# Kernel optimization log

Hardware: AMD Instinct MI355X
Metric: run time of the kernel (lower is better)

The kernel has to match this reference:

```python
import jax, jax.numpy as jnp
import numpy as np
from jax import lax

B, C, H, W = 2, 3, 512, 512
K = 8                 # kernel_size (= value_patch_size)
G = H // K            # token grid = 64
L = G * G             # 4096 tokens
FD = 128              # feature_dim
PD = C * K * K        # 192 rgb patch dim
MD = PD + FD          # 320 matching token dim
DD = 256              # matching_descriptor_dim
TOPK = 16             # attention_top_k (= reranker_top_k)
RH = 128              # reranker hidden
TEMP = 1.0
NEG = -1e9


def _to_tokens(img):
    # [B,C,H,W] -> [B,L,C*K*K], channel-major patch layout (torch unfold order)
    b = img.shape[0]
    x = img.reshape(b, C, G, K, G, K).transpose(0, 2, 4, 1, 3, 5)
    return x.reshape(b, L, PD)


def _from_tokens(tok):
    # inverse of _to_tokens (non-overlapping fold)
    b = tok.shape[0]
    x = tok.reshape(b, G, G, C, K, K).transpose(0, 3, 1, 4, 2, 5)
    return x.reshape(b, C, H, W)


def setup_inputs() -> dict:
    key = jax.random.key(0)
    ks = jax.random.split(key, 9)
    s = lambda d: 1.0 / np.sqrt(d)
    return {
        "image": jax.random.normal(ks[0], (B, C, H, W), jnp.float32),
        "features": jax.random.normal(ks[1], (B, FD, G, G), jnp.float32),
        "token_mask": jax.random.randint(ks[2], (B, L), 0, 2, jnp.int32),
        "W_desc": jax.random.normal(ks[3], (MD, DD), jnp.float32) * s(MD),
        "Wq_rr": jax.random.normal(ks[4], (MD, RH), jnp.float32) * s(MD),
        "Wk_rr": jax.random.normal(ks[5], (MD, RH), jnp.float32) * s(MD),
        "W1": jax.random.normal(ks[6], (2 * RH + 3, RH), jnp.float32) * s(2 * RH + 3),
        "b1": jnp.zeros((RH,), jnp.float32),
        "W2": jax.random.normal(ks[7], (RH, 1), jnp.float32) * s(RH),
        "b2": jnp.zeros((1,), jnp.float32),
    }


def reference(image, features, token_mask, W_desc, Wq_rr, Wk_rr, W1, b1, W2, b2):
    rgb_tok = _to_tokens(image)                                   # [B,L,192]
    feat_tok = features.reshape(B, FD, L).transpose(0, 2, 1)      # [B,L,128]
    match = jnp.concatenate([rgb_tok, feat_tok], axis=-1)          # [B,L,320]

    # stage-1 matching: descriptor GEMM + scaled dot-product logits
    desc = match @ W_desc                                          # [B,L,256]
    scale = 1.0 / (np.sqrt(DD) * TEMP)
    logits = jnp.einsum("bqd,bkd->bqk", desc, desc) * scale        # [B,L,L]
    key_invalid = token_mask.astype(logits.dtype)                  # 1 = hole
    logits = logits + NEG * key_invalid[:, None, :]

    # top-k candidate selection per query token
    top_logits, top_idx = lax.top_k(logits, TOPK)                  # [B,L,TOPK]

    gather = jax.vmap(lambda m, i: m[i])                            # per-batch gather
    cand = gather(match, top_idx)                                  # [B,L,TOPK,320]

    # relative coordinates on the token grid, normalized
    ys, xs = jnp.meshgrid(jnp.arange(G), jnp.arange(G), indexing="ij")
    pos = jnp.stack([ys.reshape(-1), xs.reshape(-1)], -1).astype(jnp.float32) / G  # [L,2]
    rel = pos[top_idx] - pos[None, :, None, :]                      # [B,L,TOPK,2]

    # reranker MLP over (query, candidate) pairs
    qf = match @ Wq_rr                                              # [B,L,RH]
    kf = cand @ Wk_rr                                               # [B,L,TOPK,RH]
    feats = jnp.concatenate(
        [qf[:, :, None, :] * kf,
         jnp.abs(qf[:, :, None, :] - kf),
         top_logits[..., None],
         rel], axis=-1)                                             # [B,L,TOPK,2RH+3]
    score = (jax.nn.gelu(feats @ W1 + b1, approximate=False) @ W2 + b2)[..., 0]
    refined = top_logits + score                                    # [B,L,TOPK]

    weights = jax.nn.softmax(refined, axis=-1)                      # [B,L,TOPK]

    # gather value patches (value_source='rgb') and blend
    vcand = gather(rgb_tok, top_idx)                                # [B,L,TOPK,192]
    out_tok = jnp.einsum("blk,blkp->blp", weights, vcand)           # [B,L,192]
    out_img = _from_tokens(out_tok)                                 # [B,C,H,W]

    # fusion_mode='replace': replace hole pixels, keep valid pixels
    pix_mask = jnp.repeat(jnp.repeat(token_mask.reshape(B, G, G), K, 1), K, 2)
    pix_mask = pix_mask[:, None, :, :]                              # [B,1,H,W]
    return jnp.where(pix_mask > 0, out_img, image)
```

## Files before the change

### kernel.cpp

```cpp
#include <hip/hip_runtime.h>
#include <hip/hip_bf16.h>
#include <math.h>

#define BB 2
#define CC 3
#define HH 512
#define WW 512
#define GG 64
#define LL 4096
#define FDIM 128
#define PDIM 192
#define MDIM 320
#define DDIM 256
#define TOPK 16
#define RHID 128
#define SCALE (1.0f/16.0f)

#define NQ2 8
#define CHK3 1024
#define KB 2
#define TOKG 16
#define TKT 32
#define NQM 4

__global__ void k_copy_init(const float* __restrict__ img, float* __restrict__ out,
                            int* __restrict__ counts) {
    int i = blockIdx.x * blockDim.x + threadIdx.x;
    if (i < 2 * BB) counts[i] = 0;
    int n4 = BB * CC * HH * WW / 4;
    const float4* s = (const float4*)img;
    float4* d = (float4*)out;
    for (int j = i; j < n4; j += gridDim.x * blockDim.x) d[j] = s[j];
}

__global__ void k_build(const float* __restrict__ img, float* __restrict__ match) {
    int bl = blockIdx.x;
    int b = bl >> 12, l = bl & (LL - 1);
    int gy = l >> 6, gx = l & 63;
    int p = threadIdx.x;
    int c = p >> 6, ky = (p >> 3) & 7, kx = p & 7;
    match[(size_t)bl * MDIM + p] =
        img[((b * CC + c) * HH + gy * 8 + ky) * WW + gx * 8 + kx];
}

__global__ __launch_bounds__(256) void k_buildf(const float* __restrict__ feat,
                                                float* __restrict__ match) {
    int b = blockIdx.y;
    int l0 = blockIdx.x * 64;
    __shared__ float tf[FDIM][65];
    int t = threadIdx.x;
    for (int idx = t; idx < FDIM * 64; idx += 256) {
        int f = idx >> 6, ll = idx & 63;
        tf[f][ll] = feat[((size_t)(b * FDIM + f) << 12) + l0 + ll];
    }
    __syncthreads();
    for (int idx = t; idx < 64 * FDIM; idx += 256) {
        int ll = idx >> 7, f = idx & 127;
        match[(size_t)(b * LL + l0 + ll) * MDIM + PDIM + f] = tf[f][ll];
    }
}

__global__ void k_compact(const int* __restrict__ mask, int* __restrict__ qlist,
                          int* __restrict__ klist, int* __restrict__ counts) {
    int bl = blockIdx.x * blockDim.x + threadIdx.x;
    if (bl >= BB * LL) return;
    int b = bl >> 12, l = bl & (LL - 1);
    if (mask[bl] > 0) {
        int s = atomicAdd(&counts[b], 1);
        qlist[b * LL + s] = l;
    } else {
        int s = atomicAdd(&counts[BB + b], 1);
        klist[b * LL + s] = l;
    }
}

__global__ __launch_bounds__(256) void k_gemm2(const float* __restrict__ match,
        const float* __restrict__ Wd, const float* __restrict__ Wq,
        const float* __restrict__ Wk,
        float* __restrict__ desc, float* __restrict__ qkf) {
    __shared__ float sm[TOKG * MDIM];
    int base = blockIdx.x * TOKG;
    int t = threadIdx.x;
    for (int i = t; i < TOKG * MDIM; i += 256) sm[i] = match[(size_t)base * MDIM + i];
    __syncthreads();
    const float4* sm4 = (const float4*)sm;
    const float* W1p = (t < 128) ? Wq : Wk;
    int c1 = t & 127;
    float acc0[TOKG], acc1[TOKG];
#pragma unroll
    for (int tt = 0; tt < TOKG; ++tt) { acc0[tt] = 0.f; acc1[tt] = 0.f; }
    for (int m = 0; m < MDIM; m += 4) {
        float w00 = Wd[(m+0)*DDIM + t], w01 = Wd[(m+1)*DDIM + t];
        float w02 = Wd[(m+2)*DDIM + t], w03 = Wd[(m+3)*DDIM + t];
        float w10 = W1p[(m+0)*RHID + c1], w11 = W1p[(m+1)*RHID + c1];
        float w12 = W1p[(m+2)*RHID + c1], w13 = W1p[(m+3)*RHID + c1];
        int mg = m >> 2;
#pragma unroll
        for (int tt = 0; tt < TOKG; ++tt) {
            float4 s = sm4[tt * (MDIM/4) + mg];
            acc0[tt] += s.x*w00 + s.y*w01 + s.z*w02 + s.w*w03;
            acc1[tt] += s.x*w10 + s.y*w11 + s.z*w12 + s.w*w13;
        }
    }
#pragma unroll
    for (int tt = 0; tt < TOKG; ++tt) {
        desc[(size_t)(base+tt)*DDIM + t] = acc0[tt];
        qkf [(size_t)(base+tt)*DDIM + t] = acc1[tt];
    }
}

__global__ __launch_bounds__(256) void k_gatherkT(const float* __restrict__ desc,
        const int* __restrict__ klist, const int* __restrict__ counts,
        float* __restrict__ kdesc_t) {
    int b = blockIdx.y;
    int vcnt = counts[BB + b];
    int kt = blockIdx.x * TKT;
    if (kt >= vcnt) return;
    int nk = min(TKT, vcnt - kt);
    __shared__ float sm[TKT][DDIM + 1];
    int t = threadIdx.x;
    for (int r = (t >> 6); r < nk; r += 4) {
        int src = klist[b * LL + kt + r];
        const float4* s = (const float4*)(desc + ((size_t)b * LL + src) * DDIM);
        float4 v = s[t & 63];
        int d0 = (t & 63) * 4;
        sm[r][d0] = v.x; sm[r][d0+1] = v.y; sm[r][d0+2] = v.z; sm[r][d0+3] = v.w;
    }
    __syncthreads();
    float* outb = kdesc_t + (size_t)b * DDIM * LL;
    int kk = t & 31;
    for (int d = (t >> 5); d < DDIM; d += 8) {
        if (kk < nk) outb[(size_t)d * LL + kt + kk] = sm[kk][d];
    }
}

__global__ __launch_bounds__(256, 4) void k_topk4(const float* __restrict__ desc,
        const float* __restrict__ kdt,
        const int* __restrict__ qlist, const int* __restrict__ klist,
        const int* __restrict__ counts,
        float* __restrict__ tval2, int* __restrict__ tidx2) {
    int b = blockIdx.z;
    int kb = blockIdx.y;
    int cnt  = counts[b];
    int vcnt = counts[BB + b];
    int i0 = blockIdx.x * NQ2;
    if (i0 >= cnt) return;
    int nq = min(NQ2, cnt - i0);
    int t = threadIdx.x;
    int lane = t & 63, w = t >> 6;

    __shared__ float sq[NQ2 * DDIM];
    __shared__ float lc[NQ2][CHK3];

#pragma unroll
    for (int qi = 0; qi < NQ2; ++qi) {
        int qtok = qlist[b * LL + i0 + min(qi, nq - 1)];
        sq[qi * DDIM + t] = desc[((size_t)b * LL + qtok) * DDIM + t];
    }
    __syncthreads();

    int khalf = (vcnt + 1) >> 1;
    int kstart = kb * khalf;
    int kend = min(vcnt, kstart + khalf);

    float tva = -INFINITY, tvb = -INFINITY;
    int   tia = 0x7fffffff, tib = 0x7fffffff;

    const float4* sq4 = (const float4*)sq;
    const float* kbase = kdt + (size_t)b * DDIM * LL;
    const int* klb = klist + b * LL;

    int nch = (kend > kstart) ? (kend - kstart + CHK3 - 1) / CHK3 : 0;
    for (int ch = 0; ch < nch; ++ch) {
        int base = kstart + ch * CHK3;
        int k0 = base + 4 * t;
        int k0c = min(k0, LL - 4);

        float acc[NQ2][4];
#pragma unroll
        for (int qi = 0; qi < NQ2; ++qi)
#pragma unroll
            for (int r = 0; r < 4; ++r) acc[qi][r] = 0.f;

#pragma unroll 2
        for (int db = 0; db < DDIM / 4; ++db) {
            float4 qv[NQ2];
#pragma unroll
            for (int qi = 0; qi < NQ2; ++qi) qv[qi] = sq4[qi * (DDIM/4) + db];
#pragma unroll
            for (int dd = 0; dd < 4; ++dd) {
                float4 kx = *(const float4*)(kbase + (size_t)(db * 4 + dd) * LL + k0c);
#pragma unroll
                for (int qi = 0; qi < NQ2; ++qi) {
                    float sv = (dd == 0) ? qv[qi].x : (dd == 1) ? qv[qi].y
                             : (dd == 2) ? qv[qi].z : qv[qi].w;
                    acc[qi][0] += sv * kx.x;
                    acc[qi][1] += sv * kx.y;
                    acc[qi][2] += sv * kx.z;
                    acc[qi][3] += sv * kx.w;
                }
            }
        }
        __syncthreads();
#pragma unroll
        for (int qi = 0; qi < NQ2; ++qi) {
            float4 o;
            o.x = (k0 + 0 < kend) ? acc[qi][0] * SCALE : -INFINITY;
            o.y = (k0 + 1 < kend) ? acc[qi][1] * SCALE : -INFINITY;
            o.z = (k0 + 2 < kend) ? acc[qi][2] * SCALE : -INFINITY;
            o.w = (k0 + 3 < kend) ? acc[qi][3] * SCALE : -INFINITY;
            *(float4*)&lc[qi][4 * t] = o;
        }
        __syncthreads();

        for (int j = 0; j < CHK3 / 64; ++j) {
            int p = j * 64 + lane;
            int gk = base + p;
            int kidx = (gk < kend) ? klb[gk] : 0x7fffffff;
            float va = lc[2 * w + 0][p];
            float vb = lc[2 * w + 1][p];
            {
                float thrv = __shfl(tva, 15);
                int   thri = __shfl(tia, 15);
                bool pass = (va > thrv) || (va == thrv && kidx < thri);
                unsigned long long mball = __ballot(pass);
                while (mball) {
                    int src = __ffsll(mball) - 1;
                    float vv = __shfl(va, src);
                    int   ii = __shfl(kidx, src);
                    bool beat = (vv > tva) || (vv == tva && ii < tia);
                    float pv = __shfl_up(tva, 1);
                    int   pi = __shfl_up(tia, 1);
                    bool beatp = (lane > 0) && ((vv > pv) || (vv == pv && ii < pi));
                    if (lane < 16 && beat) { tva = beatp ? pv : vv; tia = beatp ? pi : ii; }
                    mball &= mball - 1;
                    if (mball) {
                        float t15 = __shfl(tva, 15);
                        int   i15 = __shfl(tia, 15);
                        bool still = (va > t15) || (va == t15 && kidx < i15);
                        mball &= __ballot(still);
                    }
                }
            }
            {
                float thrv = __shfl(tvb, 15);
                int   thri = __shfl(tib, 15);
                bool pass = (vb > thrv) || (vb == thrv && kidx < thri);
                unsigned long long mball = __ballot(pass);
                while (mball) {
                    int src = __ffsll(mball) - 1;
                    float vv = __shfl(vb, src);
                    int   ii = __shfl(kidx, src);
                    bool beat = (vv > tvb) || (vv == tvb && ii < tib);
                    float pv = __shfl_up(tvb, 1);
                    int   pi = __shfl_up(tib, 1);
                    bool beatp = (lane > 0) && ((vv > pv) || (vv == pv && ii < pi));
                    if (lane < 16 && beat) { tvb = beatp ? pv : vv; tib = beatp ? pi : ii; }
                    mball &= mball - 1;
                    if (mball) {
                        float t15 = __shfl(tvb, 15);
                        int   i15 = __shfl(tib, 15);
                        bool still = (vb > t15) || (vb == t15 && kidx < i15);
                        mball &= __ballot(still);
                    }
                }
            }
        }
    }

#pragma unroll
    for (int qq = 0; qq < 2; ++qq) {
        int qi = w * 2 + qq;
        float tv = qq ? tvb : tva;
        int   ti = qq ? tib : tia;
        if (qi < nq && lane < 16) {
            size_t o = (((size_t)b * LL + i0 + qi) * KB + kb) * TOPK + lane;
            tval2[o] = tv;
            tidx2[o] = ti;
        }
    }
}

__device__ __forceinline__ float gelu_f(float x) {
    return 0.5f * x * (1.0f + erff(x * 0.70710678118654752f));
}

__global__ __launch_bounds__(256, 4) void k_mlp2(const float* __restrict__ match,
        const float* __restrict__ qkf,
        const float* __restrict__ tval2, const int* __restrict__ tidx2,
        const int* __restrict__ qlist, const int* __restrict__ counts,
        const float* __restrict__ W1, const float* __restrict__ b1,
        const float* __restrict__ W2, const float* __restrict__ b2,
        float* __restrict__ out) {
    int b = blockIdx.y;
    int cnt = counts[b];
    int i0 = blockIdx.x * NQM;
    if (i0 >= cnt) return;
    int t = threadIdx.x;
    int ql = t >> 6;
    int lane = t & 63;
    int rt = lane >> 4;
    int ht = lane & 15;
    int h0 = ht * 8;
    int k0 = rt * 4;

    __shared__ float mv[NQM][32];
    __shared__ int   mi[NQM][32];
    __shared__ float tl[NQM][16];
    __shared__ int   tix[NQM][16];
    __shared__ float rr0[NQM][16], rr1[NQM][16];
    __shared__ int   qtok[NQM];
    __shared__ float qf[NQM][128];
    __shared__ float kf[64][132];
    __shared__ float wgt[NQM][16];

    if (t < NQM) qtok[t] = qlist[b * LL + min(i0 + t, cnt - 1)];
    if (t < NQM * 32) {
        int q = t >> 5, u = t & 31;
        size_t o = (((size_t)b * LL + min(i0 + q, cnt - 1)) * KB + (u >> 4)) * TOPK + (u & 15);
        mv[q][u] = tval2[o];
        mi[q][u] = tidx2[o];
    }
    __syncthreads();
    if (t < NQM * 32) {
        int q = t >> 5, u = t & 31;
        float v = mv[q][u]; int ii = mi[q][u];
        int rank = 0;
#pragma unroll 1
        for (int x = 0; x < 32; ++x) {
            float vx = mv[q][x]; int ix = mi[q][x];
            rank += ((vx > v) || (vx == v && (ix < ii || (ix == ii && x < u)))) ? 1 : 0;
        }
        if (rank < TOPK) {
            int kidx = (ii < 0 || ii >= LL) ? 0 : ii;
            tl[q][rank] = v;
            tix[q][rank] = kidx;
            int qt = qtok[q];
            rr0[q][rank] = (float)((kidx >> 6) - (qt >> 6)) * (1.0f / GG);
            rr1[q][rank] = (float)((kidx & 63) - (qt & 63)) * (1.0f / GG);
        }
    }
    __syncthreads();
    for (int idx = t; idx < NQM * 128; idx += 256) {
        int q = idx >> 7, d = idx & 127;
        qf[q][d] = qkf[((size_t)b * LL + qtok[q]) * DDIM + d];
    }
    for (int idx = t; idx < 64 * 128; idx += 256) {
        int row = idx >> 7, d = idx & 127;
        kf[row][d] = qkf[((size_t)b * LL + tix[row >> 4][row & 15]) * DDIM + 128 + d];
    }
    __syncthreads();

    float acc[4][8];
#pragma unroll
    for (int i = 0; i < 4; ++i)
#pragma unroll
        for (int h = 0; h < 8; ++h) acc[i][h] = 0.f;

    const float4* W14 = (const float4*)W1;
    const float* qfr = qf[ql];
    const float* kfr0 = &kf[ql * 16 + k0][0];
    for (int j = 0; j < 128; ++j) {
        float qv = qfr[j];
        int ca = (j * RHID + h0) >> 2;
        int cb = ((RHID + j) * RHID + h0) >> 2;
        float4 wa0 = W14[ca], wa1 = W14[ca + 1];
        float4 wb0 = W14[cb], wb1 = W14[cb + 1];
#pragma unroll
        for (int i = 0; i < 4; ++i) {
            float kv = kfr0[i * 132 + j];
            float pa = qv * kv;
            float pb = fabsf(qv - kv);
            acc[i][0] += pa * wa0.x + pb * wb0.x;
            acc[i][1] += pa * wa0.y + pb * wb0.y;
            acc[i][2] += pa * wa0.z + pb * wb0.z;
            acc[i][3] += pa * wa0.w + pb * wb0.w;
            acc[i][4] += pa * wa1.x + pb * wb1.x;
            acc[i][5] += pa * wa1.y + pb * wb1.y;
            acc[i][6] += pa * wa1.z + pb * wb1.z;
            acc[i][7] += pa * wa1.w + pb * wb1.w;
        }
    }

    int cl = (256 * RHID + h0) >> 2;
    int cr0 = (257 * RHID + h0) >> 2;
    int cr1 = (258 * RHID + h0) >> 2;
    float4 wl0 = W14[cl], wl1 = W14[cl + 1];
    float4 wra = W14[cr0], wrb = W14[cr0 + 1];
    float4 wsa = W14[cr1], wsb = W14[cr1 + 1];
    float4 bb0 = ((const float4*)b1)[h0 >> 2], bb1v = ((const float4*)b1)[(h0 >> 2) + 1];
    float4 w20 = ((const float4*)W2)[h0 >> 2], w21 = ((const float4*)W2)[(h0 >> 2) + 1];
    float b2v = b2[0];

    float scv0, scv1, scv2, scv3;
    {
#pragma unroll
        for (int i = 0; i < 4; ++i) {
            int k = k0 + i;
            float tlv = tl[ql][k], r0v = rr0[ql][k], r1v = rr1[ql][k];
            float s = 0.f;
            s += gelu_f(acc[i][0] + tlv*wl0.x + r0v*wra.x + r1v*wsa.x + bb0.x) * w20.x;
            s += gelu_f(acc[i][1] + tlv*wl0.y + r0v*wra.y + r1v*wsa.y + bb0.y) * w20.y;
            s += gelu_f(acc[i][2] + tlv*wl0.z + r0v*wra.z + r1v*wsa.z + bb0.z) * w20.z;
            s += gelu_f(acc[i][3] + tlv*wl0.w + r0v*wra.w + r1v*wsa.w + bb0.w) * w20.w;
            s += gelu_f(acc[i][4] + tlv*wl1.x + r0v*wrb.x + r1v*wsb.x + bb1v.x) * w21.x;
            s += gelu_f(acc[i][5] + tlv*wl1.y + r0v*wrb.y + r1v*wsb.y + bb1v.y) * w21.y;
            s += gelu_f(acc[i][6] + tlv*wl1.z + r0v*wrb.z + r1v*wsb.z + bb1v.z) * w21.z;
            s += gelu_f(acc[i][7] + tlv*wl1.w + r0v*wrb.w + r1v*wsb.w + bb1v.w) * w21.w;
            s += __shfl_xor(s, 1); s += __shfl_xor(s, 2);
            s += __shfl_xor(s, 4); s += __shfl_xor(s, 8);
            if (i == 0) scv0 = s; else if (i == 1) scv1 = s;
            else if (i == 2) scv2 = s; else scv3 = s;
        }
    }
    if (ht == 0) {
        wgt[ql][k0 + 0] = scv0;
        wgt[ql][k0 + 1] = scv1;
        wgt[ql][k0 + 2] = scv2;
        wgt[ql][k0 + 3] = scv3;
    }
    __syncthreads();
    if (lane < 16) {
        float refined = tl[ql][lane] + wgt[ql][lane] + b2v;
        float m = refined;
        for (int off = 8; off > 0; off >>= 1) m = fmaxf(m, __shfl_xor(m, off, 16));
        float e = expf(refined - m);
        float s = e;
        for (int off = 8; off > 0; off >>= 1) s += __shfl_xor(s, off, 16);
        wgt[ql][lane] = e / s;
    }
    __syncthreads();
    int gyq = qtok[ql] >> 6, gxq = qtok[ql] & 63;
    for (int p = lane; p < PDIM; p += 64) {
        float o = 0.f;
#pragma unroll
        for (int k = 0; k < TOPK; ++k)
            o += wgt[ql][k] * match[((size_t)b * LL + tix[ql][k]) * MDIM + p];
        int c = p >> 6, ky = (p >> 3) & 7, kx = p & 7;
        out[((b * CC + c) * HH + gyq * 8 + ky) * WW + gxq * 8 + kx] = o;
    }
}

extern "C" void kernel_launch(void* const* d_in, const int* in_sizes, int n_in,
                              void* d_out, int out_size, void* d_ws, size_t ws_size,
                              hipStream_t stream) {
    const float* image    = (const float*)d_in[0];
    const float* features = (const float*)d_in[1];
    const int*   tmask    = (const int*)d_in[2];
    const float* W_desc   = (const float*)d_in[3];
    const float* Wq       = (const float*)d_in[4];
    const float* Wk       = (const float*)d_in[5];
    const float* W1       = (const float*)d_in[6];
    const float* b1       = (const float*)d_in[7];
    const float* W2       = (const float*)d_in[8];
    const float* b2       = (const float*)d_in[9];
    float* out = (float*)d_out;

    float* ws    = (float*)d_ws;
    float* match = ws;
    float* desc  = match + (size_t)BB * LL * MDIM;
    float* qkf   = desc  + (size_t)BB * LL * DDIM;
    float* kdt   = qkf   + (size_t)BB * LL * DDIM;
    float* tval2 = kdt   + (size_t)BB * DDIM * LL;
    int*   tidx2 = (int*)(tval2 + (size_t)BB * LL * KB * TOPK);
    int*   qlist = tidx2 + (size_t)BB * LL * KB * TOPK;
    int*   klist = qlist + BB * LL;
    int*   counts = klist + BB * LL;

    k_copy_init<<<1024, 256, 0, stream>>>(image, out, counts);
    k_build<<<BB * LL, PDIM, 0, stream>>>(image, match);
    k_buildf<<<dim3(LL / 64, BB), 256, 0, stream>>>(features, match);
    k_compact<<<(BB * LL + 255) / 256, 256, 0, stream>>>(tmask, qlist, klist, counts);
    k_gemm2<<<BB * LL / TOKG, 256, 0, stream>>>(match, W_desc, Wq, Wk, desc, qkf);
    k_gatherkT<<<dim3(LL / TKT, BB), 256, 0, stream>>>(desc, klist, counts, kdt);
    k_topk4<<<dim3(LL / NQ2, KB, BB), 256, 0, stream>>>(desc, kdt, qlist, klist,
                                                        counts, tval2, tidx2);
    k_mlp2<<<dim3(LL / NQM, BB), 256, 0, stream>>>(match, qkf, tval2, tidx2, qlist,
                                                   counts, W1, b1, W2, b2, out);
}
```

Measured before the change: 405.9 us.

## Split projection GEMM across 512 threads, interleave top-k insert loops, unroll MLP loop

The fused projection GEMM now launches 512 threads per block, each computing a single output column (desc, Wq or Wk) instead of two. This halves accumulator registers per thread and doubles thread-level parallelism. The top-k kernel now runs the two per-query ballot insertion loops in one combined loop, so the two queries' shuffle chains can overlap. The MLP inner loop gets an unroll-2 pragma. The column computation contains a redundant, overwritten expression, and the larger block may lower occupancy.

```diff
diff --git a/kernel.cpp b/kernel.cpp
--- a/kernel.cpp
+++ b/kernel.cpp
@@ -74,38 +74,45 @@
     }
 }
 
-__global__ __launch_bounds__(256) void k_gemm2(const float* __restrict__ match,
+__global__ __launch_bounds__(512) void k_gemm3(const float* __restrict__ match,
         const float* __restrict__ Wd, const float* __restrict__ Wq,
         const float* __restrict__ Wk,
         float* __restrict__ desc, float* __restrict__ qkf) {
     __shared__ float sm[TOKG * MDIM];
     int base = blockIdx.x * TOKG;
     int t = threadIdx.x;
-    for (int i = t; i < TOKG * MDIM; i += 256) sm[i] = match[(size_t)base * MDIM + i];
+    for (int i = t; i < TOKG * MDIM; i += 512) sm[i] = match[(size_t)base * MDIM + i];
     __syncthreads();
     const float4* sm4 = (const float4*)sm;
-    const float* W1p = (t < 128) ? Wq : Wk;
-    int c1 = t & 127;
-    float acc0[TOKG], acc1[TOKG];
-#pragma unroll
-    for (int tt = 0; tt < TOKG; ++tt) { acc0[tt] = 0.f; acc1[tt] = 0.f; }
+    const float* Wp;
+    int ld, c;
+    if (t < 256)      { Wp = Wd; ld = DDIM; c = t; }
+    else if (t < 384) { Wp = Wq; ld = RHID; c = t - 256; }
+    else              { Wp = Wk; ld = RHID; c = t - 384; }
+    float acc[TOKG];
+#pragma unroll
+    for (int tt = 0; tt < TOKG; ++tt) acc[tt] = 0.f;
     for (int m = 0; m < MDIM; m += 4) {
-        float w00 = Wd[(m+0)*DDIM + t], w01 = Wd[(m+1)*DDIM + t];
-        float w02 = Wd[(m+2)*DDIM + t], w03 = Wd[(m+3)*DDIM + t];
-        float w10 = W1p[(m+0)*RHID + c1], w11 = W1p[(m+1)*RHID + c1];
-        float w12 = W1p[(m+2)*RHID + c1], w13 = W1p[(m+3)*RHID + c1];
+        float w0 = Wp[(m+0)*ld + c], w1 = Wp[(m+1)*ld + c];
+        float w2 = Wp[(m+2)*ld + c], w3 = Wp[(m+3)*ld + c];
         int mg = m >> 2;
 #pragma unroll
         for (int tt = 0; tt < TOKG; ++tt) {
             float4 s = sm4[tt * (MDIM/4) + mg];
-            acc0[tt] += s.x*w00 + s.y*w01 + s.z*w02 + s.w*w03;
-            acc1[tt] += s.x*w10 + s.y*w11 + s.z*w12 + s.w*w13;
-        }
-    }
-#pragma unroll
-    for (int tt = 0; tt < TOKG; ++tt) {
-        desc[(size_t)(base+tt)*DDIM + t] = acc0[tt];
-        qkf [(size_t)(base+tt)*DDIM + t] = acc1[tt];
+            acc[tt] += s.x*w0 + s.y*w1 + s.z*w2 + s.w*w3;
+        }
+    }
+    if (t < 256) {
+#pragma unroll
+        for (int tt = 0; tt < TOKG; ++tt)
+            desc[(size_t)(base+tt)*DDIM + t] = acc[tt];
+    } else {
+        int qc = t - 256;
+        int col = (t < 384) ? qc : (qc + RHID - RHID) + RHID * 0 + (t - 384) + RHID;
+        col = (t < 384) ? (t - 256) : (t - 384 + RHID);
+#pragma unroll
+        for (int tt = 0; tt < TOKG; ++tt)
+            qkf[(size_t)(base+tt)*DDIM + col] = acc[tt];
     }
 }
 
@@ -219,13 +226,14 @@
             int kidx = (gk < kend) ? klb[gk] : 0x7fffffff;
             float va = lc[2 * w + 0][p];
             float vb = lc[2 * w + 1][p];
-            {
-                float thrv = __shfl(tva, 15);
-                int   thri = __shfl(tia, 15);
-                bool pass = (va > thrv) || (va == thrv && kidx < thri);
-                unsigned long long mball = __ballot(pass);
-                while (mball) {
-                    int src = __ffsll(mball) - 1;
+            float thrv; int thri;
+            thrv = __shfl(tva, 15); thri = __shfl(tia, 15);
+            unsigned long long mA = __ballot((va > thrv) || (va == thrv && kidx < thri));
+            thrv = __shfl(tvb, 15); thri = __shfl(tib, 15);
+            unsigned long long mB = __ballot((vb > thrv) || (vb == thrv && kidx < thri));
+            while (mA | mB) {
+                if (mA) {
+                    int src = __ffsll(mA) - 1;
                     float vv = __shfl(va, src);
                     int   ii = __shfl(kidx, src);
                     bool beat = (vv > tva) || (vv == tva && ii < tia);
@@ -233,22 +241,15 @@
                     int   pi = __shfl_up(tia, 1);
                     bool beatp = (lane > 0) && ((vv > pv) || (vv == pv && ii < pi));
                     if (lane < 16 && beat) { tva = beatp ? pv : vv; tia = beatp ? pi : ii; }
-                    mball &= mball - 1;
-                    if (mball) {
+                    mA &= mA - 1;
+                    if (mA) {
                         float t15 = __shfl(tva, 15);
                         int   i15 = __shfl(tia, 15);
-                        bool still = (va > t15) || (va == t15 && kidx < i15);
-                        mball &= __ballot(still);
+                        mA &= __ballot((va > t15) || (va == t15 && kidx < i15));
                     }
                 }
-            }
-            {
-                float thrv = __shfl(tvb, 15);
-                int   thri = __shfl(tib, 15);
-                bool pass = (vb > thrv) || (vb == thrv && kidx < thri);
-                unsigned long long mball = __ballot(pass);
-                while (mball) {
-                    int src = __ffsll(mball) - 1;
+                if (mB) {
+                    int src = __ffsll(mB) - 1;
                     float vv = __shfl(vb, src);
                     int   ii = __shfl(kidx, src);
                     bool beat = (vv > tvb) || (vv == tvb && ii < tib);
@@ -256,12 +257,11 @@
                     int   pi = __shfl_up(tib, 1);
                     bool beatp = (lane > 0) && ((vv > pv) || (vv == pv && ii < pi));
                     if (lane < 16 && beat) { tvb = beatp ? pv : vv; tib = beatp ? pi : ii; }
-                    mball &= mball - 1;
-                    if (mball) {
+                    mB &= mB - 1;
+                    if (mB) {
                         float t15 = __shfl(tvb, 15);
                         int   i15 = __shfl(tib, 15);
-                        bool still = (vb > t15) || (vb == t15 && kidx < i15);
-                        mball &= __ballot(still);
+                        mB &= __ballot((vb > t15) || (vb == t15 && kidx < i15));
                     }
                 }
             }
@@ -360,6 +360,7 @@
     const float4* W14 = (const float4*)W1;
     const float* qfr = qf[ql];
     const float* kfr0 = &kf[ql * 16 + k0][0];
+#pragma unroll 2
     for (int j = 0; j < 128; ++j) {
         float qv = qfr[j];
         int ca = (j * RHID + h0) >> 2;
@@ -471,7 +472,7 @@
     k_build<<<BB * LL, PDIM, 0, stream>>>(image, match);
     k_buildf<<<dim3(LL / 64, BB), 256, 0, stream>>>(features, match);
     k_compact<<<(BB * LL + 255) / 256, 256, 0, stream>>>(tmask, qlist, klist, counts);
-    k_gemm2<<<BB * LL / TOKG, 256, 0, stream>>>(match, W_desc, Wq, Wk, desc, qkf);
+    k_gemm3<<<BB * LL / TOKG, 512, 0, stream>>>(match, W_desc, Wq, Wk, desc, qkf);
     k_gatherkT<<<dim3(LL / TKT, BB), 256, 0, stream>>>(desc, klist, counts, kdt);
     k_topk4<<<dim3(LL / NQ2, KB, BB), 256, 0, stream>>>(desc, kdt, qlist, klist,
                                                         counts, tval2, tidx2);
```

Measured after the change: 424.1 us. +4.5%, slower.
